# Optimization experiments

Measured on AMD Instinct MI355X. Metric: run time of the kernel, lower is better.

The kernel has to match this reference:

```python
import jax, jax.numpy as jnp
import numpy as np

EMBED = 192
HEADS = 6
WIN = (7, 7, 7)
B = 256
NW = 64  # number of distinct window masks; b // NW = true batch
N = WIN[0] * WIN[1] * WIN[2]  # 343 tokens per window


def _rel_pos_index(win):
    # Faithful port of the torch buffer construction.
    coords = np.stack(np.meshgrid(np.arange(win[0]), np.arange(win[1]), np.arange(win[2]), indexing='ij'))
    cf = coords.reshape(3, -1)                     # [3, N]
    rel = cf[:, :, None] - cf[:, None, :]          # [3, N, N]
    rel = rel.transpose(1, 2, 0).copy()            # [N, N, 3]
    rel[..., 0] += win[0] - 1
    rel[..., 1] += win[1] - 1
    rel[..., 2] += win[2] - 1
    rel[..., 0] *= (2 * win[1] - 1) * (2 * win[2] - 1)
    rel[..., 1] *= (2 * win[2] - 1)
    return rel.sum(-1).astype(np.int32)            # [N, N]


def setup_inputs() -> dict:
    key = jax.random.key(0)
    ks = jax.random.split(key, 8)
    table_size = (2 * WIN[0] - 1) * (2 * WIN[1] - 1) * (2 * WIN[2] - 1)  # 2197
    return {
        'x_in': jax.random.normal(ks[0], (B, N, EMBED), dtype=jnp.float32),
        'x_cross': jax.random.normal(ks[1], (B, N, EMBED), dtype=jnp.float32),
        'mask': jnp.zeros((NW, N, N), dtype=jnp.float32),
        'q_w': jax.random.normal(ks[2], (EMBED, EMBED), dtype=jnp.float32) * 0.02,
        'kv_w': jax.random.normal(ks[3], (2 * EMBED, EMBED), dtype=jnp.float32) * 0.02,
        'proj_w': jax.random.normal(ks[4], (EMBED, EMBED), dtype=jnp.float32) * 0.02,
        'proj_b': jnp.zeros((EMBED,), dtype=jnp.float32),
        'bias_table': jax.random.normal(ks[5], (table_size, HEADS), dtype=jnp.float32) * 0.02,
        'rel_idx': jnp.asarray(_rel_pos_index(WIN)),
    }


def reference(x_in, x_cross, mask, q_w, kv_w, proj_w, proj_b, bias_table, rel_idx):
    b, n, c = x_in.shape
    h = HEADS
    hd = c // h
    scale = hd ** -0.5
    # Projections (torch Linear: y = x @ W^T), no qkv bias
    q = (x_in @ q_w.T).reshape(b, n, h, hd).transpose(0, 2, 1, 3) * scale   # [b,h,n,hd]
    kv = (x_cross @ kv_w.T).reshape(b, n, 2, h, hd)
    k = kv[:, :, 0].transpose(0, 2, 1, 3)                                   # [b,h,n,hd]
    v = kv[:, :, 1].transpose(0, 2, 1, 3)                                   # [b,h,n,hd]
    attn = jnp.einsum('bhqd,bhkd->bhqk', q, k)                              # [b,h,n,n]
    # Gathered relative position bias
    bias = bias_table[rel_idx[:n, :n].reshape(-1)].reshape(n, n, h).transpose(2, 0, 1)
    attn = attn + bias[None]
    # Window mask add: [b//nw, nw, h, n, n] + [1, nw, 1, n, n]
    nw = mask.shape[0]
    attn = attn.reshape(b // nw, nw, h, n, n) + mask[None, :, None]
    attn = attn.reshape(b, h, n, n)
    attn = jax.nn.softmax(attn, axis=-1)
    x = jnp.einsum('bhqk,bhkd->bhqd', attn, v).transpose(0, 2, 1, 3).reshape(b, n, c)
    return x @ proj_w.T + proj_b
```

## Files before the change

### kernel.cpp

```cpp
#include <hip/hip_runtime.h>

#define NTOK 343
#define NPAD 352
#define CEMB 192
#define NH   6
#define HD   32
#define NB   256
#define NWIN 64
#define FPLANE 123904

typedef __attribute__((ext_vector_type(8))) short short8;
typedef __attribute__((ext_vector_type(4))) float f32x4;
typedef __attribute__((ext_vector_type(4))) unsigned int uint4v;
typedef __attribute__((ext_vector_type(2))) unsigned int uint2v;

__device__ __forceinline__ unsigned short f2bf(float f) {
    unsigned int u = __builtin_bit_cast(unsigned int, f);
    u += 0x7fffu + ((u >> 16) & 1u);
    return (unsigned short)(u >> 16);
}
__device__ __forceinline__ float bf2f(unsigned short h) {
    unsigned int u = ((unsigned int)h) << 16;
    return __builtin_bit_cast(float, u);
}
__device__ __forceinline__ short8 pack8(float4 f0, float4 f1) {
    short8 r;
    r[0] = (short)f2bf(f0.x); r[1] = (short)f2bf(f0.y);
    r[2] = (short)f2bf(f0.z); r[3] = (short)f2bf(f0.w);
    r[4] = (short)f2bf(f1.x); r[5] = (short)f2bf(f1.y);
    r[6] = (short)f2bf(f1.z); r[7] = (short)f2bf(f1.w);
    return r;
}
__device__ __forceinline__ unsigned int cvt_pk_bf16(float lo, float hi) {
    unsigned int r;
    asm("v_cvt_pk_bf16_f32 %0, %1, %2" : "=v"(r) : "v"(lo), "v"(hi));
    return r;
}

#define LOG2E 1.4426950408889634f

__global__ void prep_weights(const float* __restrict__ qw, const float* __restrict__ kvw,
                             const float* __restrict__ pw,
                             unsigned short* __restrict__ qwb, unsigned short* __restrict__ kvwb,
                             unsigned short* __restrict__ pwb) {
    const float scale = 0.17677669529663689f * LOG2E;
    int idx = blockIdx.x * 256 + threadIdx.x;
    if (idx < 36864)        qwb[idx] = f2bf(qw[idx] * scale);
    else if (idx < 110592)  kvwb[idx - 36864] = f2bf(kvw[idx - 36864]);
    else if (idx < 147456)  pwb[idx - 110592] = f2bf(pw[idx - 110592]);
}

__global__ void prep_biasF(const float* __restrict__ table, const int* __restrict__ rel,
                           unsigned short* __restrict__ biasF) {
    int idx = blockIdx.x * 256 + threadIdx.x;
    int lane = idx & 63;
    int rest = idx >> 6;
    int t = rest & 1; rest >>= 1;
    int ch = rest % 11; rest /= 11;
    int mt = rest % 22; int h = rest / 22;
    int q = mt * 16 + (lane & 15);
    int k0 = ch * 32 + t * 16 + ((lane >> 4) << 2);
    ushort4 out;
#pragma unroll
    for (int r = 0; r < 4; r++) {
        int k = k0 + r;
        float v = (q < NTOK && k < NTOK) ? table[rel[q * NTOK + k] * NH + h] * LOG2E : 0.f;
        ((unsigned short*)&out)[r] = f2bf(v);
    }
    *(ushort4*)(biasF + (size_t)idx * 4) = out;
}

__global__ void prep_maskF(const float* __restrict__ mask, unsigned short* __restrict__ maskF) {
    int idx = blockIdx.x * 256 + threadIdx.x;
    int lane = idx & 63;
    int rest = idx >> 6;
    int t = rest & 1; rest >>= 1;
    int ch = rest % 11; rest /= 11;
    int mt = rest % 22; int w = rest / 22;
    int q = mt * 16 + (lane & 15);
    int k0 = ch * 32 + t * 16 + ((lane >> 4) << 2);
    ushort4 out;
#pragma unroll
    for (int r = 0; r < 4; r++) {
        int k = k0 + r;
        float v;
        if (k >= NTOK) v = -60000.f;
        else if (q < NTOK) v = mask[((size_t)w * NTOK + q) * NTOK + k] * LOG2E;
        else v = 0.f;
        ((unsigned short*)&out)[r] = f2bf(v);
    }
    *(ushort4*)(maskF + (size_t)idx * 4) = out;
}

__global__ __launch_bounds__(512, 2)
void qkv_q_kernel(const float* __restrict__ x_in, const unsigned short* __restrict__ qwb,
                  unsigned short* __restrict__ Qb) {
    extern __shared__ char smem[];
    unsigned short* Ws = (unsigned short*)smem;
    const int tid = threadIdx.x;
    const int wave = tid >> 6, lane = tid & 63;
    const int quad = lane >> 4, l16 = lane & 15;
    const int b = blockIdx.x;
    const f32x4 zero4 = {0.f, 0.f, 0.f, 0.f};

    for (int i = tid; i < 4608; i += 512) {
        int r = i / 24, c8 = i - r * 24;
        *(short8*)(Ws + r * 200 + c8 * 8) = *(const short8*)(qwb + (size_t)r * CEMB + c8 * 8);
    }
    __syncthreads();

    for (int mi = 0; mi < 3; mi++) {
        int mt = wave + (mi << 3);
        if (mt >= 22) continue;
        int row = mt * 16 + l16;
        f32x4 acc[12];
#pragma unroll
        for (int nt = 0; nt < 12; nt++) acc[nt] = zero4;
#pragma unroll
        for (int kc = 0; kc < 6; kc++) {
            short8 a = {};
            if (row < NTOK) {
                const float* xp = x_in + ((size_t)b * NTOK + row) * CEMB + kc * 32 + (quad << 3);
                a = pack8(*(const float4*)xp, *(const float4*)(xp + 4));
            }
#pragma unroll
            for (int nt = 0; nt < 12; nt++) {
                const short8 bf = *(const short8*)(Ws + (nt * 16 + l16) * 200 + kc * 32 + (quad << 3));
                acc[nt] = __builtin_amdgcn_mfma_f32_16x16x32_bf16(a, bf, acc[nt], 0, 0, 0);
            }
        }
        unsigned short* dst = Qb + (size_t)b * NPAD * CEMB;
#pragma unroll
        for (int nt = 0; nt < 12; nt++) {
#pragma unroll
            for (int r = 0; r < 4; r++) {
                int m = mt * 16 + (quad << 2) + r;
                dst[(size_t)m * CEMB + nt * 16 + l16] = f2bf(acc[nt][r]);
            }
        }
    }
}

__global__ __launch_bounds__(512, 2)
void qkv_kv_kernel(const float* __restrict__ x_cross, const unsigned short* __restrict__ kvwb,
                   unsigned short* __restrict__ Kb, unsigned short* __restrict__ Vtb) {
    extern __shared__ char smem[];
    unsigned short* Ws = (unsigned short*)smem;
    const int tid = threadIdx.x;
    const int wave = tid >> 6, lane = tid & 63;
    const int quad = lane >> 4, l16 = lane & 15;
    const int b = blockIdx.x;
    const f32x4 zero4 = {0.f, 0.f, 0.f, 0.f};

    for (int i = tid; i < 4608; i += 512) {
        int r = i / 24, c8 = i - r * 24;
        *(short8*)(Ws + r * 200 + c8 * 8) = *(const short8*)(kvwb + (size_t)r * CEMB + c8 * 8);
    }

    short8 a[3][6];
#pragma unroll
    for (int mi = 0; mi < 3; mi++) {
        int mt = wave + (mi << 3);
        int row = mt * 16 + l16;
#pragma unroll
        for (int kc = 0; kc < 6; kc++) {
            a[mi][kc] = (short8){};
            if (mt < 22 && row < NTOK) {
                const float* xp = x_cross + ((size_t)b * NTOK + row) * CEMB + kc * 32 + (quad << 3);
                a[mi][kc] = pack8(*(const float4*)xp, *(const float4*)(xp + 4));
            }
        }
    }
    __syncthreads();

#pragma unroll
    for (int mi = 0; mi < 3; mi++) {
        int mt = wave + (mi << 3);
        if (mt >= 22) continue;
        f32x4 acc[12];
#pragma unroll
        for (int nt = 0; nt < 12; nt++) acc[nt] = zero4;
#pragma unroll
        for (int kc = 0; kc < 6; kc++) {
#pragma unroll
            for (int nt = 0; nt < 12; nt++) {
                const short8 bf = *(const short8*)(Ws + (nt * 16 + l16) * 200 + kc * 32 + (quad << 3));
                acc[nt] = __builtin_amdgcn_mfma_f32_16x16x32_bf16(a[mi][kc], bf, acc[nt], 0, 0, 0);
            }
        }
        unsigned short* dst = Kb + (size_t)b * NPAD * CEMB;
#pragma unroll
        for (int nt = 0; nt < 12; nt++) {
#pragma unroll
            for (int r = 0; r < 4; r++) {
                int m = mt * 16 + (quad << 2) + r;
                dst[(size_t)m * CEMB + nt * 16 + l16] = f2bf(acc[nt][r]);
            }
        }
    }
    __syncthreads();
    for (int i = tid; i < 4608; i += 512) {
        int r = i / 24, c8 = i - r * 24;
        *(short8*)(Ws + r * 200 + c8 * 8) = *(const short8*)(kvwb + (size_t)(192 + r) * CEMB + c8 * 8);
    }
    __syncthreads();

#pragma unroll
    for (int mi = 0; mi < 3; mi++) {
        int mt = wave + (mi << 3);
        if (mt >= 22) continue;
        f32x4 acc[12];
#pragma unroll
        for (int nt = 0; nt < 12; nt++) acc[nt] = zero4;
#pragma unroll
        for (int kc = 0; kc < 6; kc++) {
#pragma unroll
            for (int nt = 0; nt < 12; nt++) {
                const short8 bf = *(const short8*)(Ws + (nt * 16 + l16) * 200 + kc * 32 + (quad << 3));
                acc[nt] = __builtin_amdgcn_mfma_f32_16x16x32_bf16(a[mi][kc], bf, acc[nt], 0, 0, 0);
            }
        }
#pragma unroll
        for (int nt = 0; nt < 12; nt++) {
            int h = nt >> 1, d = ((nt & 1) << 4) + l16;
#pragma unroll
            for (int r = 0; r < 4; r++) {
                int m = mt * 16 + (quad << 2) + r;
                Vtb[(((size_t)b * NH + h) * 32 + d) * 360 + m] = f2bf(acc[nt][r]);
            }
        }
    }
}

__global__ __launch_bounds__(512, 6)
void attn_kernel(const unsigned short* __restrict__ Qb, const unsigned short* __restrict__ Kb,
                 const unsigned short* __restrict__ Vtb,
                 const unsigned short* __restrict__ biasF, const unsigned short* __restrict__ maskF,
                 unsigned short* __restrict__ attnb) {
    extern __shared__ char smem[];
    unsigned short* Ks = (unsigned short*)smem;
    unsigned short* Vt = (unsigned short*)(smem + 28160);

    const int tid = threadIdx.x;
    const int wave = tid >> 6, lane = tid & 63;
    const int quad = lane >> 4, l16 = lane & 15;
    const int q4 = quad << 2, q8 = quad << 3;
    const int p = blockIdx.x;
    const int L = (p & 7) * 192 + (p >> 3);
    const int w = L / 24, r_ = L - w * 24;
    const int b = (r_ / 6) * 64 + w;
    const int h = r_ - (r_ / 6) * 6;
    const f32x4 zero4 = {0.f, 0.f, 0.f, 0.f};

    for (int i = tid; i < 1408; i += 512) {
        int key = i >> 2, part = i & 3;
        *(short8*)(Ks + key * 40 + part * 8) =
            *(const short8*)(Kb + ((size_t)b * NPAD + key) * CEMB + h * 32 + part * 8);
    }
    const unsigned short* vsrc = Vtb + (size_t)(b * NH + h) * 32 * 360;
    for (int i = tid; i < 1440; i += 512) {
        *(short8*)(Vt + i * 8) = *(const short8*)(vsrc + i * 8);
    }
    short8 qa[3] = {};
#pragma unroll
    for (int i = 0; i < 3; i++) {
        int mt = wave + (i << 3);
        if (mt < 22)
            qa[i] = *(const short8*)(Qb + ((size_t)b * NPAD + mt * 16 + l16) * CEMB + h * 32 + q8);
    }
    __syncthreads();

    const unsigned short* bF = biasF + (size_t)h * FPLANE;
    const unsigned short* mF = maskF + (size_t)w * FPLANE;
    const int lane4 = lane << 2;
#pragma unroll
    for (int i = 0; i < 3; i++) {
        int mt = wave + (i << 3);
        if (mt >= 22) continue;
        float rp = 0.f;
        f32x4 o0 = zero4, o1 = zero4;
        int off = mt * 5632;
        ushort4 bt0c = *(const ushort4*)(bF + off + lane4);
        ushort4 mk0c = *(const ushort4*)(mF + off + lane4);
        ushort4 bt1c = *(const ushort4*)(bF + off + 256 + lane4);
        ushort4 mk1c = *(const ushort4*)(mF + off + 256 + lane4);
        for (int ch = 0; ch < 11; ch++) {
            const int kb_ = ch * 32;
            const int offn = (ch < 10) ? off + 512 : off;
            ushort4 bt0n = *(const ushort4*)(bF + offn + lane4);
            ushort4 mk0n = *(const ushort4*)(mF + offn + lane4);
            ushort4 bt1n = *(const ushort4*)(bF + offn + 256 + lane4);
            ushort4 mk1n = *(const ushort4*)(mF + offn + 256 + lane4);
            f32x4 c0, c1;
            c0[0] = bf2f(bt0c.x) + bf2f(mk0c.x);
            c0[1] = bf2f(bt0c.y) + bf2f(mk0c.y);
            c0[2] = bf2f(bt0c.z) + bf2f(mk0c.z);
            c0[3] = bf2f(bt0c.w) + bf2f(mk0c.w);
            c1[0] = bf2f(bt1c.x) + bf2f(mk1c.x);
            c1[1] = bf2f(bt1c.y) + bf2f(mk1c.y);
            c1[2] = bf2f(bt1c.z) + bf2f(mk1c.z);
            c1[3] = bf2f(bt1c.w) + bf2f(mk1c.w);
            const short8 k0f = *(const short8*)(Ks + (kb_ + l16) * 40 + q8);
            const short8 k1f = *(const short8*)(Ks + (kb_ + 16 + l16) * 40 + q8);
            f32x4 s0 = __builtin_amdgcn_mfma_f32_16x16x32_bf16(k0f, qa[i], c0, 0, 0, 0);
            f32x4 s1 = __builtin_amdgcn_mfma_f32_16x16x32_bf16(k1f, qa[i], c1, 0, 0, 0);
            float p00 = __builtin_amdgcn_exp2f(s0[0]);
            float p01 = __builtin_amdgcn_exp2f(s0[1]);
            float p02 = __builtin_amdgcn_exp2f(s0[2]);
            float p03 = __builtin_amdgcn_exp2f(s0[3]);
            float p10 = __builtin_amdgcn_exp2f(s1[0]);
            float p11 = __builtin_amdgcn_exp2f(s1[1]);
            float p12 = __builtin_amdgcn_exp2f(s1[2]);
            float p13 = __builtin_amdgcn_exp2f(s1[3]);
            rp += ((p00 + p01) + (p02 + p03)) + ((p10 + p11) + (p12 + p13));
            unsigned int e0 = cvt_pk_bf16(p00, p01);
            unsigned int e1 = cvt_pk_bf16(p02, p03);
            unsigned int e2 = cvt_pk_bf16(p10, p11);
            unsigned int e3 = cvt_pk_bf16(p12, p13);
            uint2v sa = __builtin_amdgcn_permlane32_swap(e0, e2, false, false);
            uint2v sb = __builtin_amdgcn_permlane32_swap(e1, e3, false, false);
            uint2v ta = __builtin_amdgcn_permlane16_swap(sa[0], sa[1], false, false);
            uint2v tb = __builtin_amdgcn_permlane16_swap(sb[0], sb[1], false, false);
            const short8 pa = __builtin_bit_cast(short8, (uint4v){ta[0], tb[0], ta[1], tb[1]});
            const short8 v0 = *(const short8*)(Vt + l16 * 360 + kb_ + q8);
            const short8 v1 = *(const short8*)(Vt + (16 + l16) * 360 + kb_ + q8);
            o0 = __builtin_amdgcn_mfma_f32_16x16x32_bf16(pa, v0, o0, 0, 0, 0);
            o1 = __builtin_amdgcn_mfma_f32_16x16x32_bf16(pa, v1, o1, 0, 0, 0);
            bt0c = bt0n; mk0c = mk0n; bt1c = bt1n; mk1c = mk1n;
            off = offn;
        }
        rp += __shfl_xor(rp, 16);
        rp += __shfl_xor(rp, 32);
        float inv = 1.f / rp;
#pragma unroll
        for (int r = 0; r < 4; r++) {
            float invr = __shfl(inv, (lane & 48) | (q4 + r));
            int n = mt * 16 + q4 + r;
            if (n < NTOK) {
                size_t base = ((size_t)b * NTOK + n) * CEMB + h * 32;
                attnb[base + l16] = f2bf(o0[r] * invr);
                attnb[base + 16 + l16] = f2bf(o1[r] * invr);
            }
        }
    }
}

__global__ __launch_bounds__(512, 2)
void proj_kernel(const unsigned short* __restrict__ attnb, const unsigned short* __restrict__ pwb,
                 const float* __restrict__ proj_b, float* __restrict__ out) {
    extern __shared__ char smem[];
    unsigned short* Ws = (unsigned short*)smem;
    const int tid = threadIdx.x;
    const int wave = tid >> 6, lane = tid & 63;
    const int quad = lane >> 4, l16 = lane & 15;
    for (int i = tid; i < 4608; i += 512) {
        int r = i / 24, c8 = i - r * 24;
        *(short8*)(Ws + r * 200 + c8 * 8) = *(const short8*)(pwb + (size_t)r * CEMB + c8 * 8);
    }
    float pb[12];
#pragma unroll
    for (int nt = 0; nt < 12; nt++) pb[nt] = proj_b[nt * 16 + l16];
    __syncthreads();

    const int mt = blockIdx.x * 8 + wave;
    const f32x4 zero4 = {0.f, 0.f, 0.f, 0.f};
    f32x4 acc[12];
#pragma unroll
    for (int nt = 0; nt < 12; nt++) acc[nt] = zero4;
#pragma unroll
    for (int ks = 0; ks < 6; ks++) {
        const short8 a = *(const short8*)(attnb + ((size_t)mt * 16 + l16) * CEMB + ks * 32 + (quad << 3));
#pragma unroll
        for (int nt = 0; nt < 12; nt++) {
            const short8 bfrag = *(const short8*)(Ws + (nt * 16 + l16) * 200 + ks * 32 + (quad << 3));
            acc[nt] = __builtin_amdgcn_mfma_f32_16x16x32_bf16(a, bfrag, acc[nt], 0, 0, 0);
        }
    }
#pragma unroll
    for (int nt = 0; nt < 12; nt++) {
#pragma unroll
        for (int r = 0; r < 4; r++) {
            int m = mt * 16 + (quad << 2) + r;
            out[(size_t)m * CEMB + nt * 16 + l16] = acc[nt][r] + pb[nt];
        }
    }
}

extern "C" void kernel_launch(void* const* d_in, const int* in_sizes, int n_in,
                              void* d_out, int out_size, void* d_ws, size_t ws_size,
                              hipStream_t stream) {
    (void)in_sizes; (void)n_in; (void)out_size; (void)ws_size;
    const float* x_in    = (const float*)d_in[0];
    const float* x_cross = (const float*)d_in[1];
    const float* mask    = (const float*)d_in[2];
    const float* q_w     = (const float*)d_in[3];
    const float* kv_w    = (const float*)d_in[4];
    const float* proj_w  = (const float*)d_in[5];
    const float* proj_b  = (const float*)d_in[6];
    const float* btab    = (const float*)d_in[7];
    const int*   rel     = (const int*)d_in[8];
    float* out = (float*)d_out;
    char* ws = (char*)d_ws;

    unsigned short* qwb   = (unsigned short*)(ws + 0);
    unsigned short* kvwb  = (unsigned short*)(ws + 73728);
    unsigned short* pwb   = (unsigned short*)(ws + 221184);
    unsigned short* biasF = (unsigned short*)(ws + 294912);
    unsigned short* maskF = (unsigned short*)(ws + 1781760);
    unsigned short* attnb = (unsigned short*)(ws + 17641472);
    unsigned short* Qb    = (unsigned short*)(ws + 51359744);
    unsigned short* Kb    = (unsigned short*)(ws + 85962752);
    unsigned short* Vtb   = (unsigned short*)(ws + 120565760);

    prep_weights<<<576, 256, 0, stream>>>(q_w, kv_w, proj_w, qwb, kvwb, pwb);
    prep_biasF<<<728, 256, 0, stream>>>(btab, rel, biasF);
    prep_maskF<<<7744, 256, 0, stream>>>(mask, maskF);
    qkv_q_kernel<<<NB, 512, 76800, stream>>>(x_in, qwb, Qb);
    qkv_kv_kernel<<<NB, 512, 76800, stream>>>(x_cross, kvwb, Kb, Vtb);
    attn_kernel<<<NB * NH, 512, 51200, stream>>>(Qb, Kb, Vtb, biasF, maskF, attnb);
    proj_kernel<<<686, 512, 76800, stream>>>(attnb, pwb, proj_b, out);
}
```

Measured before the change: 367.0 us.

## Merge prep and QKV launches, read V from global, raise attention occupancy

Merges the weight and bias prep kernels into one launch and the Q and KV projection kernels into one grid of 2*NB blocks, so fewer launches run and the two projections can execute concurrently. In the attention kernel, V is no longer staged in shared memory; it is read directly from global memory, which drops LDS per block to 28160 bytes, and launch bounds are raised to 8 blocks per CU. Q fragments are now loaded per tile and the bias+mask sum is computed one chunk ahead. The trade is more global/L2 traffic for V and possibly register pressure at the higher occupancy target.

Measured after the change: 405.6 us. 10.5% more time.

```diff
diff --git a/kernel.cpp b/kernel.cpp
--- a/kernel.cpp
+++ b/kernel.cpp
@@ -39,35 +39,35 @@
 
 #define LOG2E 1.4426950408889634f
 
-__global__ void prep_weights(const float* __restrict__ qw, const float* __restrict__ kvw,
-                             const float* __restrict__ pw,
-                             unsigned short* __restrict__ qwb, unsigned short* __restrict__ kvwb,
-                             unsigned short* __restrict__ pwb) {
-    const float scale = 0.17677669529663689f * LOG2E;
-    int idx = blockIdx.x * 256 + threadIdx.x;
-    if (idx < 36864)        qwb[idx] = f2bf(qw[idx] * scale);
-    else if (idx < 110592)  kvwb[idx - 36864] = f2bf(kvw[idx - 36864]);
-    else if (idx < 147456)  pwb[idx - 110592] = f2bf(pw[idx - 110592]);
-}
-
-__global__ void prep_biasF(const float* __restrict__ table, const int* __restrict__ rel,
-                           unsigned short* __restrict__ biasF) {
-    int idx = blockIdx.x * 256 + threadIdx.x;
-    int lane = idx & 63;
-    int rest = idx >> 6;
-    int t = rest & 1; rest >>= 1;
-    int ch = rest % 11; rest /= 11;
-    int mt = rest % 22; int h = rest / 22;
-    int q = mt * 16 + (lane & 15);
-    int k0 = ch * 32 + t * 16 + ((lane >> 4) << 2);
-    ushort4 out;
-#pragma unroll
-    for (int r = 0; r < 4; r++) {
-        int k = k0 + r;
-        float v = (q < NTOK && k < NTOK) ? table[rel[q * NTOK + k] * NH + h] * LOG2E : 0.f;
-        ((unsigned short*)&out)[r] = f2bf(v);
-    }
-    *(ushort4*)(biasF + (size_t)idx * 4) = out;
+__global__ void prep_wb(const float* __restrict__ qw, const float* __restrict__ kvw,
+                        const float* __restrict__ pw, const float* __restrict__ table,
+                        const int* __restrict__ rel,
+                        unsigned short* __restrict__ qwb, unsigned short* __restrict__ kvwb,
+                        unsigned short* __restrict__ pwb, unsigned short* __restrict__ biasF) {
+    if (blockIdx.x < 576) {
+        const float scale = 0.17677669529663689f * LOG2E;
+        int idx = blockIdx.x * 256 + threadIdx.x;
+        if (idx < 36864)        qwb[idx] = f2bf(qw[idx] * scale);
+        else if (idx < 110592)  kvwb[idx - 36864] = f2bf(kvw[idx - 36864]);
+        else if (idx < 147456)  pwb[idx - 110592] = f2bf(pw[idx - 110592]);
+    } else {
+        int idx = (blockIdx.x - 576) * 256 + threadIdx.x;
+        int lane = idx & 63;
+        int rest = idx >> 6;
+        int t = rest & 1; rest >>= 1;
+        int ch = rest % 11; rest /= 11;
+        int mt = rest % 22; int h = rest / 22;
+        int q = mt * 16 + (lane & 15);
+        int k0 = ch * 32 + t * 16 + ((lane >> 4) << 2);
+        ushort4 out;
+#pragma unroll
+        for (int r = 0; r < 4; r++) {
+            int k = k0 + r;
+            float v = (q < NTOK && k < NTOK) ? table[rel[q * NTOK + k] * NH + h] * LOG2E : 0.f;
+            ((unsigned short*)&out)[r] = f2bf(v);
+        }
+        *(ushort4*)(biasF + (size_t)idx * 4) = out;
+    }
 }
 
 __global__ void prep_maskF(const float* __restrict__ mask, unsigned short* __restrict__ maskF) {
@@ -93,153 +93,141 @@
 }
 
 __global__ __launch_bounds__(512, 2)
-void qkv_q_kernel(const float* __restrict__ x_in, const unsigned short* __restrict__ qwb,
-                  unsigned short* __restrict__ Qb) {
+void qkv_kernel(const float* __restrict__ x_in, const float* __restrict__ x_cross,
+                const unsigned short* __restrict__ qwb, const unsigned short* __restrict__ kvwb,
+                unsigned short* __restrict__ Qb, unsigned short* __restrict__ Kb,
+                unsigned short* __restrict__ Vtb) {
     extern __shared__ char smem[];
     unsigned short* Ws = (unsigned short*)smem;
     const int tid = threadIdx.x;
     const int wave = tid >> 6, lane = tid & 63;
     const int quad = lane >> 4, l16 = lane & 15;
-    const int b = blockIdx.x;
     const f32x4 zero4 = {0.f, 0.f, 0.f, 0.f};
 
-    for (int i = tid; i < 4608; i += 512) {
-        int r = i / 24, c8 = i - r * 24;
-        *(short8*)(Ws + r * 200 + c8 * 8) = *(const short8*)(qwb + (size_t)r * CEMB + c8 * 8);
-    }
-    __syncthreads();
-
-    for (int mi = 0; mi < 3; mi++) {
-        int mt = wave + (mi << 3);
-        if (mt >= 22) continue;
-        int row = mt * 16 + l16;
-        f32x4 acc[12];
-#pragma unroll
-        for (int nt = 0; nt < 12; nt++) acc[nt] = zero4;
-#pragma unroll
-        for (int kc = 0; kc < 6; kc++) {
-            short8 a = {};
-            if (row < NTOK) {
-                const float* xp = x_in + ((size_t)b * NTOK + row) * CEMB + kc * 32 + (quad << 3);
-                a = pack8(*(const float4*)xp, *(const float4*)(xp + 4));
-            }
+    if (blockIdx.x < NB) {
+        const int b = blockIdx.x;
+        for (int i = tid; i < 4608; i += 512) {
+            int r = i / 24, c8 = i - r * 24;
+            *(short8*)(Ws + r * 200 + c8 * 8) = *(const short8*)(qwb + (size_t)r * CEMB + c8 * 8);
+        }
+        __syncthreads();
+        for (int mi = 0; mi < 3; mi++) {
+            int mt = wave + (mi << 3);
+            if (mt >= 22) continue;
+            int row = mt * 16 + l16;
+            f32x4 acc[12];
+#pragma unroll
+            for (int nt = 0; nt < 12; nt++) acc[nt] = zero4;
+#pragma unroll
+            for (int kc = 0; kc < 6; kc++) {
+                short8 a = {};
+                if (row < NTOK) {
+                    const float* xp = x_in + ((size_t)b * NTOK + row) * CEMB + kc * 32 + (quad << 3);
+                    a = pack8(*(const float4*)xp, *(const float4*)(xp + 4));
+                }
+#pragma unroll
+                for (int nt = 0; nt < 12; nt++) {
+                    const short8 bf = *(const short8*)(Ws + (nt * 16 + l16) * 200 + kc * 32 + (quad << 3));
+                    acc[nt] = __builtin_amdgcn_mfma_f32_16x16x32_bf16(a, bf, acc[nt], 0, 0, 0);
+                }
+            }
+            unsigned short* dst = Qb + (size_t)b * NPAD * CEMB;
 #pragma unroll
             for (int nt = 0; nt < 12; nt++) {
-                const short8 bf = *(const short8*)(Ws + (nt * 16 + l16) * 200 + kc * 32 + (quad << 3));
-                acc[nt] = __builtin_amdgcn_mfma_f32_16x16x32_bf16(a, bf, acc[nt], 0, 0, 0);
-            }
-        }
-        unsigned short* dst = Qb + (size_t)b * NPAD * CEMB;
-#pragma unroll
-        for (int nt = 0; nt < 12; nt++) {
-#pragma unroll
-            for (int r = 0; r < 4; r++) {
-                int m = mt * 16 + (quad << 2) + r;
-                dst[(size_t)m * CEMB + nt * 16 + l16] = f2bf(acc[nt][r]);
-            }
-        }
-    }
-}
-
-__global__ __launch_bounds__(512, 2)
-void qkv_kv_kernel(const float* __restrict__ x_cross, const unsigned short* __restrict__ kvwb,
-                   unsigned short* __restrict__ Kb, unsigned short* __restrict__ Vtb) {
-    extern __shared__ char smem[];
-    unsigned short* Ws = (unsigned short*)smem;
-    const int tid = threadIdx.x;
-    const int wave = tid >> 6, lane = tid & 63;
-    const int quad = lane >> 4, l16 = lane & 15;
-    const int b = blockIdx.x;
-    const f32x4 zero4 = {0.f, 0.f, 0.f, 0.f};
-
-    for (int i = tid; i < 4608; i += 512) {
-        int r = i / 24, c8 = i - r * 24;
-        *(short8*)(Ws + r * 200 + c8 * 8) = *(const short8*)(kvwb + (size_t)r * CEMB + c8 * 8);
-    }
-
-    short8 a[3][6];
-#pragma unroll
-    for (int mi = 0; mi < 3; mi++) {
-        int mt = wave + (mi << 3);
-        int row = mt * 16 + l16;
-#pragma unroll
-        for (int kc = 0; kc < 6; kc++) {
-            a[mi][kc] = (short8){};
-            if (mt < 22 && row < NTOK) {
-                const float* xp = x_cross + ((size_t)b * NTOK + row) * CEMB + kc * 32 + (quad << 3);
-                a[mi][kc] = pack8(*(const float4*)xp, *(const float4*)(xp + 4));
-            }
-        }
-    }
-    __syncthreads();
-
-#pragma unroll
-    for (int mi = 0; mi < 3; mi++) {
-        int mt = wave + (mi << 3);
-        if (mt >= 22) continue;
-        f32x4 acc[12];
-#pragma unroll
-        for (int nt = 0; nt < 12; nt++) acc[nt] = zero4;
-#pragma unroll
-        for (int kc = 0; kc < 6; kc++) {
+#pragma unroll
+                for (int r = 0; r < 4; r++) {
+                    int m = mt * 16 + (quad << 2) + r;
+                    dst[(size_t)m * CEMB + nt * 16 + l16] = f2bf(acc[nt][r]);
+                }
+            }
+        }
+    } else {
+        const int b = blockIdx.x - NB;
+        for (int i = tid; i < 4608; i += 512) {
+            int r = i / 24, c8 = i - r * 24;
+            *(short8*)(Ws + r * 200 + c8 * 8) = *(const short8*)(kvwb + (size_t)r * CEMB + c8 * 8);
+        }
+        short8 a[3][6];
+#pragma unroll
+        for (int mi = 0; mi < 3; mi++) {
+            int mt = wave + (mi << 3);
+            int row = mt * 16 + l16;
+#pragma unroll
+            for (int kc = 0; kc < 6; kc++) {
+                a[mi][kc] = (short8){};
+                if (mt < 22 && row < NTOK) {
+                    const float* xp = x_cross + ((size_t)b * NTOK + row) * CEMB + kc * 32 + (quad << 3);
+                    a[mi][kc] = pack8(*(const float4*)xp, *(const float4*)(xp + 4));
+                }
+            }
+        }
+        __syncthreads();
+#pragma unroll
+        for (int mi = 0; mi < 3; mi++) {
+            int mt = wave + (mi << 3);
+            if (mt >= 22) continue;
+            f32x4 acc[12];
+#pragma unroll
+            for (int nt = 0; nt < 12; nt++) acc[nt] = zero4;
+#pragma unroll
+            for (int kc = 0; kc < 6; kc++) {
+#pragma unroll
+                for (int nt = 0; nt < 12; nt++) {
+                    const short8 bf = *(const short8*)(Ws + (nt * 16 + l16) * 200 + kc * 32 + (quad << 3));
+                    acc[nt] = __builtin_amdgcn_mfma_f32_16x16x32_bf16(a[mi][kc], bf, acc[nt], 0, 0, 0);
+                }
+            }
+            unsigned short* dst = Kb + (size_t)b * NPAD * CEMB;
 #pragma unroll
             for (int nt = 0; nt < 12; nt++) {
-                const short8 bf = *(const short8*)(Ws + (nt * 16 + l16) * 200 + kc * 32 + (quad << 3));
-                acc[nt] = __builtin_amdgcn_mfma_f32_16x16x32_bf16(a[mi][kc], bf, acc[nt], 0, 0, 0);
-            }
-        }
-        unsigned short* dst = Kb + (size_t)b * NPAD * CEMB;
-#pragma unroll
-        for (int nt = 0; nt < 12; nt++) {
-#pragma unroll
-            for (int r = 0; r < 4; r++) {
-                int m = mt * 16 + (quad << 2) + r;
-                dst[(size_t)m * CEMB + nt * 16 + l16] = f2bf(acc[nt][r]);
-            }
-        }
-    }
-    __syncthreads();
-    for (int i = tid; i < 4608; i += 512) {
-        int r = i / 24, c8 = i - r * 24;
-        *(short8*)(Ws + r * 200 + c8 * 8) = *(const short8*)(kvwb + (size_t)(192 + r) * CEMB + c8 * 8);
-    }
-    __syncthreads();
-
-#pragma unroll
-    for (int mi = 0; mi < 3; mi++) {
-        int mt = wave + (mi << 3);
-        if (mt >= 22) continue;
-        f32x4 acc[12];
-#pragma unroll
-        for (int nt = 0; nt < 12; nt++) acc[nt] = zero4;
-#pragma unroll
-        for (int kc = 0; kc < 6; kc++) {
+#pragma unroll
+                for (int r = 0; r < 4; r++) {
+                    int m = mt * 16 + (quad << 2) + r;
+                    dst[(size_t)m * CEMB + nt * 16 + l16] = f2bf(acc[nt][r]);
+                }
+            }
+        }
+        __syncthreads();
+        for (int i = tid; i < 4608; i += 512) {
+            int r = i / 24, c8 = i - r * 24;
+            *(short8*)(Ws + r * 200 + c8 * 8) = *(const short8*)(kvwb + (size_t)(192 + r) * CEMB + c8 * 8);
+        }
+        __syncthreads();
+#pragma unroll
+        for (int mi = 0; mi < 3; mi++) {
+            int mt = wave + (mi << 3);
+            if (mt >= 22) continue;
+            f32x4 acc[12];
+#pragma unroll
+            for (int nt = 0; nt < 12; nt++) acc[nt] = zero4;
+#pragma unroll
+            for (int kc = 0; kc < 6; kc++) {
+#pragma unroll
+                for (int nt = 0; nt < 12; nt++) {
+                    const short8 bf = *(const short8*)(Ws + (nt * 16 + l16) * 200 + kc * 32 + (quad << 3));
+                    acc[nt] = __builtin_amdgcn_mfma_f32_16x16x32_bf16(a[mi][kc], bf, acc[nt], 0, 0, 0);
+                }
+            }
 #pragma unroll
             for (int nt = 0; nt < 12; nt++) {
-                const short8 bf = *(const short8*)(Ws + (nt * 16 + l16) * 200 + kc * 32 + (quad << 3));
-                acc[nt] = __builtin_amdgcn_mfma_f32_16x16x32_bf16(a[mi][kc], bf, acc[nt], 0, 0, 0);
-            }
-        }
-#pragma unroll
-        for (int nt = 0; nt < 12; nt++) {
-            int h = nt >> 1, d = ((nt & 1) << 4) + l16;
-#pragma unroll
-            for (int r = 0; r < 4; r++) {
-                int m = mt * 16 + (quad << 2) + r;
-                Vtb[(((size_t)b * NH + h) * 32 + d) * 360 + m] = f2bf(acc[nt][r]);
-            }
-        }
-    }
-}
-
-__global__ __launch_bounds__(512, 6)
+                int h = nt >> 1, d = ((nt & 1) << 4) + l16;
+#pragma unroll
+                for (int r = 0; r < 4; r++) {
+                    int m = mt * 16 + (quad << 2) + r;
+                    Vtb[(((size_t)b * NH + h) * 32 + d) * 360 + m] = f2bf(acc[nt][r]);
+                }
+            }
+        }
+    }
+}
+
+__global__ __launch_bounds__(512, 8)
 void attn_kernel(const unsigned short* __restrict__ Qb, const unsigned short* __restrict__ Kb,
                  const unsigned short* __restrict__ Vtb,
                  const unsigned short* __restrict__ biasF, const unsigned short* __restrict__ maskF,
                  unsigned short* __restrict__ attnb) {
     extern __shared__ char smem[];
     unsigned short* Ks = (unsigned short*)smem;
-    unsigned short* Vt = (unsigned short*)(smem + 28160);
 
     const int tid = threadIdx.x;
     const int wave = tid >> 6, lane = tid & 63;
@@ -257,33 +245,32 @@
         *(short8*)(Ks + key * 40 + part * 8) =
             *(const short8*)(Kb + ((size_t)b * NPAD + key) * CEMB + h * 32 + part * 8);
     }
-    const unsigned short* vsrc = Vtb + (size_t)(b * NH + h) * 32 * 360;
-    for (int i = tid; i < 1440; i += 512) {
-        *(short8*)(Vt + i * 8) = *(const short8*)(vsrc + i * 8);
-    }
-    short8 qa[3] = {};
-#pragma unroll
-    for (int i = 0; i < 3; i++) {
-        int mt = wave + (i << 3);
-        if (mt < 22)
-            qa[i] = *(const short8*)(Qb + ((size_t)b * NPAD + mt * 16 + l16) * CEMB + h * 32 + q8);
-    }
     __syncthreads();
 
+    const unsigned short* Vp = Vtb + (size_t)(b * NH + h) * 32 * 360;
     const unsigned short* bF = biasF + (size_t)h * FPLANE;
     const unsigned short* mF = maskF + (size_t)w * FPLANE;
     const int lane4 = lane << 2;
+
 #pragma unroll
     for (int i = 0; i < 3; i++) {
         int mt = wave + (i << 3);
         if (mt >= 22) continue;
+        const short8 qa = *(const short8*)(Qb + ((size_t)b * NPAD + mt * 16 + l16) * CEMB + h * 32 + q8);
         float rp = 0.f;
         f32x4 o0 = zero4, o1 = zero4;
         int off = mt * 5632;
-        ushort4 bt0c = *(const ushort4*)(bF + off + lane4);
-        ushort4 mk0c = *(const ushort4*)(mF + off + lane4);
-        ushort4 bt1c = *(const ushort4*)(bF + off + 256 + lane4);
-        ushort4 mk1c = *(const ushort4*)(mF + off + 256 + lane4);
+        f32x4 c0c, c1c;
+        {
+            ushort4 bt0 = *(const ushort4*)(bF + off + lane4);
+            ushort4 mk0 = *(const ushort4*)(mF + off + lane4);
+            ushort4 bt1 = *(const ushort4*)(bF + off + 256 + lane4);
+            ushort4 mk1 = *(const ushort4*)(mF + off + 256 + lane4);
+            c0c[0] = bf2f(bt0.x) + bf2f(mk0.x); c0c[1] = bf2f(bt0.y) + bf2f(mk0.y);
+            c0c[2] = bf2f(bt0.z) + bf2f(mk0.z); c0c[3] = bf2f(bt0.w) + bf2f(mk0.w);
+            c1c[0] = bf2f(bt1.x) + bf2f(mk1.x); c1c[1] = bf2f(bt1.y) + bf2f(mk1.y);
+            c1c[2] = bf2f(bt1.z) + bf2f(mk1.z); c1c[3] = bf2f(bt1.w) + bf2f(mk1.w);
+        }
         for (int ch = 0; ch < 11; ch++) {
             const int kb_ = ch * 32;
             const int offn = (ch < 10) ? off + 512 : off;
@@ -291,19 +278,15 @@
             ushort4 mk0n = *(const ushort4*)(mF + offn + lane4);
             ushort4 bt1n = *(const ushort4*)(bF + offn + 256 + lane4);
             ushort4 mk1n = *(const ushort4*)(mF + offn + 256 + lane4);
-            f32x4 c0, c1;
-            c0[0] = bf2f(bt0c.x) + bf2f(mk0c.x);
-            c0[1] = bf2f(bt0c.y) + bf2f(mk0c.y);
-            c0[2] = bf2f(bt0c.z) + bf2f(mk0c.z);
-            c0[3] = bf2f(bt0c.w) + bf2f(mk0c.w);
-            c1[0] = bf2f(bt1c.x) + bf2f(mk1c.x);
-            c1[1] = bf2f(bt1c.y) + bf2f(mk1c.y);
-            c1[2] = bf2f(bt1c.z) + bf2f(mk1c.z);
-            c1[3] = bf2f(bt1c.w) + bf2f(mk1c.w);
+            f32x4 c0n, c1n;
+            c0n[0] = bf2f(bt0n.x) + bf2f(mk0n.x); c0n[1] = bf2f(bt0n.y) + bf2f(mk0n.y);
+            c0n[2] = bf2f(bt0n.z) + bf2f(mk0n.z); c0n[3] = bf2f(bt0n.w) + bf2f(mk0n.w);
+            c1n[0] = bf2f(bt1n.x) + bf2f(mk1n.x); c1n[1] = bf2f(bt1n.y) + bf2f(mk1n.y);
+            c1n[2] = bf2f(bt1n.z) + bf2f(mk1n.z); c1n[3] = bf2f(bt1n.w) + bf2f(mk1n.w);
             const short8 k0f = *(const short8*)(Ks + (kb_ + l16) * 40 + q8);
             const short8 k1f = *(const short8*)(Ks + (kb_ + 16 + l16) * 40 + q8);
-            f32x4 s0 = __builtin_amdgcn_mfma_f32_16x16x32_bf16(k0f, qa[i], c0, 0, 0, 0);
-            f32x4 s1 = __builtin_amdgcn_mfma_f32_16x16x32_bf16(k1f, qa[i], c1, 0, 0, 0);
+            f32x4 s0 = __builtin_amdgcn_mfma_f32_16x16x32_bf16(k0f, qa, c0c, 0, 0, 0);
+            f32x4 s1 = __builtin_amdgcn_mfma_f32_16x16x32_bf16(k1f, qa, c1c, 0, 0, 0);
             float p00 = __builtin_amdgcn_exp2f(s0[0]);
             float p01 = __builtin_amdgcn_exp2f(s0[1]);
             float p02 = __builtin_amdgcn_exp2f(s0[2]);
@@ -322,12 +305,11 @@
             uint2v ta = __builtin_amdgcn_permlane16_swap(sa[0], sa[1], false, false);
             uint2v tb = __builtin_amdgcn_permlane16_swap(sb[0], sb[1], false, false);
             const short8 pa = __builtin_bit_cast(short8, (uint4v){ta[0], tb[0], ta[1], tb[1]});
-            const short8 v0 = *(const short8*)(Vt + l16 * 360 + kb_ + q8);
-            const short8 v1 = *(const short8*)(Vt + (16 + l16) * 360 + kb_ + q8);
+            const short8 v0 = *(const short8*)(Vp + l16 * 360 + kb_ + q8);
+            const short8 v1 = *(const short8*)(Vp + (16 + l16) * 360 + kb_ + q8);
             o0 = __builtin_amdgcn_mfma_f32_16x16x32_bf16(pa, v0, o0, 0, 0, 0);
             o1 = __builtin_amdgcn_mfma_f32_16x16x32_bf16(pa, v1, o1, 0, 0, 0);
-            bt0c = bt0n; mk0c = mk0n; bt1c = bt1n; mk1c = mk1n;
-            off = offn;
+            c0c = c0n; c1c = c1n; off = offn;
         }
         rp += __shfl_xor(rp, 16);
         rp += __shfl_xor(rp, 32);
@@ -412,11 +394,9 @@
     unsigned short* Kb    = (unsigned short*)(ws + 85962752);
     unsigned short* Vtb   = (unsigned short*)(ws + 120565760);
 
-    prep_weights<<<576, 256, 0, stream>>>(q_w, kv_w, proj_w, qwb, kvwb, pwb);
-    prep_biasF<<<728, 256, 0, stream>>>(btab, rel, biasF);
+    prep_wb<<<1304, 256, 0, stream>>>(q_w, kv_w, proj_w, btab, rel, qwb, kvwb, pwb, biasF);
     prep_maskF<<<7744, 256, 0, stream>>>(mask, maskF);
-    qkv_q_kernel<<<NB, 512, 76800, stream>>>(x_in, qwb, Qb);
-    qkv_kv_kernel<<<NB, 512, 76800, stream>>>(x_cross, kvwb, Kb, Vtb);
-    attn_kernel<<<NB * NH, 512, 51200, stream>>>(Qb, Kb, Vtb, biasF, maskF, attnb);
+    qkv_kernel<<<2 * NB, 512, 76800, stream>>>(x_in, x_cross, qwb, kvwb, Qb, Kb, Vtb);
+    attn_kernel<<<NB * NH, 512, 28160, stream>>>(Qb, Kb, Vtb, biasF, maskF, attnb);
     proj_kernel<<<686, 512, 76800, stream>>>(attnb, pwb, proj_b, out);
 }
```
